# Kernel optimization log

Measured on AMD Instinct MI355X. Metric: run time of the kernel, lower is better.

## Reference

```python
import jax, jax.numpy as jnp
import numpy as np

KERNEL_MUL = 2.0
KERNEL_NUM = 5


def setup_inputs() -> dict:
    key = jax.random.key(0)
    k1, k2 = jax.random.split(key)
    source = jax.random.normal(k1, (4096, 256), dtype=jnp.float32)
    target = jax.random.normal(k2, (4096, 256), dtype=jnp.float32)
    return {"source": source, "target": target}


def _gaussian_mmd(source, target):
    n_src = source.shape[0]
    total = jnp.concatenate([source, target], axis=0)  # [n, d]
    n = total.shape[0]
    # pairwise squared L2 distances via the GEMM trick (equivalent to the
    # expand-based (total0 - total1)**2 sum in the original)
    sq = jnp.sum(total * total, axis=1)  # [n]
    l2 = jnp.maximum(sq[:, None] + sq[None, :] - 2.0 * (total @ total.T), 0.0)  # [n, n]
    # bandwidth from detached distances (torch uses .data -> stop_gradient)
    bandwidth = jax.lax.stop_gradient(jnp.sum(l2)) / (n * n - n)
    bandwidth = bandwidth / (KERNEL_MUL ** (KERNEL_NUM // 2))
    # multi-bandwidth gaussian kernel sum
    kernels = jnp.zeros_like(l2)
    for i in range(KERNEL_NUM):
        kernels = kernels + jnp.exp(-l2 / (bandwidth * KERNEL_MUL ** i))
    xx = jnp.mean(kernels[:n_src, :n_src])
    yy = jnp.mean(kernels[n_src:, n_src:])
    xy = jnp.mean(kernels[:n_src, n_src:])
    yx = jnp.mean(kernels[n_src:, :n_src])
    return xx + yy - xy - yx


def reference(source, target):
    return _gaussian_mmd(source, target)
```

## Files before the change

### kernel.cpp

```cpp
#include <hip/hip_runtime.h>

typedef float f32x4 __attribute__((ext_vector_type(4)));
typedef short bf16x8 __attribute__((ext_vector_type(8)));

#define N_TOTAL 8192
#define N_SRC   4096
#define DDIM    256
#define LOG2E   1.4426950408889634f

__device__ __forceinline__ unsigned short f2bf(float f) {
  return __builtin_bit_cast(unsigned short, (__bf16)f);
}

__global__ __launch_bounds__(256) void k_sq_cast(
    const float* __restrict__ src, const float* __restrict__ tgt,
    float* __restrict__ sq, unsigned short* __restrict__ Vbf,
    float* __restrict__ colsum) {
  const int t = threadIdx.x;
  const int lane = t & 63;
  const int w = t >> 6;
  const int row = blockIdx.x * 4 + w;
  const float* rowp = (row < N_SRC) ? (src + (size_t)row * DDIM)
                                    : (tgt + (size_t)(row - N_SRC) * DDIM);
  float4 v = ((const float4*)rowp)[lane];
  float ss = v.x * v.x + v.y * v.y + v.z * v.z + v.w * v.w;
  #pragma unroll
  for (int m = 32; m >= 1; m >>= 1) ss += __shfl_xor(ss, m, 64);
  if (lane == 0) sq[row] = ss;
  ushort4 p;
  p.x = f2bf(v.x); p.y = f2bf(v.y); p.z = f2bf(v.z); p.w = f2bf(v.w);
  ((ushort4*)Vbf)[(size_t)row * 64 + lane] = p;
  if (blockIdx.x == 0) colsum[t] = 0.0f;
}

__global__ __launch_bounds__(256) void k_colsum(
    const float* __restrict__ src, const float* __restrict__ tgt,
    float* __restrict__ colsum) {
  const int t = threadIdx.x;
  const int b = blockIdx.x;
  const float* base = (b < 32) ? (src + (size_t)b * 128 * DDIM)
                               : (tgt + (size_t)(b - 32) * 128 * DDIM);
  float p = 0.0f;
  for (int r = 0; r < 128; ++r) p += base[(size_t)r * DDIM + t];
  atomicAdd(colsum + t, p);
}

__global__ __launch_bounds__(256) void k_bw(
    const float* __restrict__ sq, const float* __restrict__ colsum,
    float* __restrict__ nc0, double* __restrict__ accum) {
  const int t = threadIdx.x;
  const int lane = t & 63;
  const int w = t >> 6;
  float sp = 0.0f;
  for (int i = t; i < N_TOTAL; i += 256) sp += sq[i];
  float c = colsum[t];
  float cp = c * c;
  #pragma unroll
  for (int m = 32; m >= 1; m >>= 1) {
    sp += __shfl_xor(sp, m, 64);
    cp += __shfl_xor(cp, m, 64);
  }
  __shared__ float red[8];
  if (lane == 0) { red[w] = sp; red[4 + w] = cp; }
  __syncthreads();
  if (t == 0) {
    float S   = red[0] + red[1] + red[2] + red[3];
    float CSQ = red[4] + red[5] + red[6] + red[7];
    float sum_l2 = 2.0f * (float)N_TOTAL * S - 2.0f * CSQ;
    float bw = sum_l2 / ((float)N_TOTAL * (float)N_TOTAL - (float)N_TOTAL) / 4.0f;
    *nc0 = -LOG2E / bw;
    *accum = 0.0;
  }
}

__global__ __launch_bounds__(256) void k_main(
    const unsigned short* __restrict__ Vbf, const float* __restrict__ sq,
    const float* __restrict__ nc0p, double* __restrict__ accum) {
  const int bcol = blockIdx.x;
  const int brow = blockIdx.y;
  if (bcol < brow) return;

  const int t = threadIdx.x;
  const int lane = t & 63;
  const int w = t >> 6;
  const int wr = w >> 1;
  const int wc = w & 1;
  const int i0 = brow * 128;
  const int j0 = bcol * 128;

  __shared__ uint4 lds4[2048];
  char* As = (char*)lds4;
  char* Bs = (char*)lds4 + 16384;

  const unsigned short* VA = Vbf + (size_t)i0 * DDIM;
  const unsigned short* VB = Vbf + (size_t)j0 * DDIM;

  f32x4 acc[4][4] = {};

  const int srow = t >> 3;
  const int scb  = (t & 7) * 16;

  for (int ks = 0; ks < 4; ++ks) {
    const int kc = ks * 64;
    __syncthreads();
    #pragma unroll
    for (int it = 0; it < 4; ++it) {
      const int r = it * 32 + srow;
      const int dst = r * 128 + (scb ^ ((r & 7) << 4));
      uint4 ga = *(const uint4*)(VA + (size_t)r * DDIM + kc + (scb >> 1));
      uint4 gb = *(const uint4*)(VB + (size_t)r * DDIM + kc + (scb >> 1));
      *(uint4*)(As + dst) = ga;
      *(uint4*)(Bs + dst) = gb;
    }
    __syncthreads();
    #pragma unroll
    for (int kk = 0; kk < 2; ++kk) {
      const int kbyte = kk * 64 + ((lane >> 4) << 4);
      bf16x8 a[4], b[4];
      #pragma unroll
      for (int m = 0; m < 4; ++m) {
        const int ra = wr * 64 + m * 16 + (lane & 15);
        a[m] = *(const bf16x8*)(As + ra * 128 + (kbyte ^ ((ra & 7) << 4)));
        const int rb = wc * 64 + m * 16 + (lane & 15);
        b[m] = *(const bf16x8*)(Bs + rb * 128 + (kbyte ^ ((rb & 7) << 4)));
      }
      #pragma unroll
      for (int m = 0; m < 4; ++m)
        #pragma unroll
        for (int n = 0; n < 4; ++n)
          acc[m][n] = __builtin_amdgcn_mfma_f32_16x16x32_bf16(a[m], b[n], acc[m][n], 0, 0, 0);
    }
  }

  const float nc0 = *nc0p;
  float rsv[16];
  const int rbase = i0 + wr * 64 + ((lane >> 4) << 2);
  #pragma unroll
  for (int m = 0; m < 4; ++m) {
    const float4 q = *(const float4*)(sq + rbase + m * 16);
    rsv[m * 4 + 0] = q.x; rsv[m * 4 + 1] = q.y;
    rsv[m * 4 + 2] = q.z; rsv[m * 4 + 3] = q.w;
  }
  float cs[4];
  const int cbase = j0 + wc * 64 + (lane & 15);
  #pragma unroll
  for (int n = 0; n < 4; ++n) cs[n] = sq[cbase + n * 16];

  float ksum = 0.0f;
  #pragma unroll
  for (int m = 0; m < 4; ++m)
    #pragma unroll
    for (int n = 0; n < 4; ++n)
      #pragma unroll
      for (int r = 0; r < 4; ++r) {
        const float g  = acc[m][n][r];
        const float l2 = fmaxf(fmaf(-2.0f, g, rsv[m * 4 + r]) + cs[n], 0.0f);
        const float tt = l2 * nc0;
        ksum += __builtin_amdgcn_exp2f(tt)
              + __builtin_amdgcn_exp2f(tt * 0.5f)
              + __builtin_amdgcn_exp2f(tt * 0.25f)
              + __builtin_amdgcn_exp2f(tt * 0.125f)
              + __builtin_amdgcn_exp2f(tt * 0.0625f);
      }

  #pragma unroll
  for (int m = 32; m >= 1; m >>= 1) ksum += __shfl_xor(ksum, m, 64);
  __shared__ float red[4];
  if (lane == 0) red[w] = ksum;
  __syncthreads();
  if (t == 0) {
    const float sign = ((brow < 32) == (bcol < 32)) ? 1.0f : -1.0f;
    const float mult = (brow == bcol) ? 1.0f : 2.0f;
    const double contrib = (double)((red[0] + red[1] + red[2] + red[3]) * sign * mult);
    atomicAdd(accum, contrib);
  }
}

__global__ void k_final(const double* __restrict__ accum, float* __restrict__ out) {
  out[0] = (float)(accum[0] * (1.0 / 16777216.0));
}

extern "C" void kernel_launch(void* const* d_in, const int* in_sizes, int n_in,
                              void* d_out, int out_size, void* d_ws, size_t ws_size,
                              hipStream_t stream) {
  const float* src = (const float*)d_in[0];
  const float* tgt = (const float*)d_in[1];
  char* ws = (char*)d_ws;
  double* accum          = (double*)ws;
  float*  nc0            = (float*)(ws + 8);
  float*  colsum         = (float*)(ws + 64);
  float*  sq             = (float*)(ws + 2048);
  unsigned short* Vbf    = (unsigned short*)(ws + 65536);
  float* out = (float*)d_out;

  hipLaunchKernelGGL(k_sq_cast, dim3(2048), dim3(256), 0, stream, src, tgt, sq, Vbf, colsum);
  hipLaunchKernelGGL(k_colsum,  dim3(64),   dim3(256), 0, stream, src, tgt, colsum);
  hipLaunchKernelGGL(k_bw,      dim3(1),    dim3(256), 0, stream, sq, colsum, nc0, accum);
  hipLaunchKernelGGL(k_main,    dim3(64, 64), dim3(256), 0, stream, Vbf, sq, nc0, accum);
  hipLaunchKernelGGL(k_final,   dim3(1),    dim3(1),   0, stream, accum, out);
}
```

Before: 133.8 us.

## Fuse prep kernels, compact triangular grid, square-chain exps, last-block finalize

Merges the square-norm/cast, column-sum and bandwidth kernels into one 64-block prep kernel that writes per-block column partials. Each main block now recomputes the bandwidth redundantly from those partials and sq. The main grid launches only the 2080 upper-triangle tiles, mapping block id to row and column with a sqrt formula. The five exp2 calls become one exp2 followed by repeated squaring. A done counter lets the last block write the output, which removes the final kernel. This cuts launch count, idle blocks and transcendental work, at the cost of redundant per-block reductions and a small change in rounding from the squaring chain.

Result: slower. 171.2 us (+27.9%).

```diff
diff --git a/kernel.cpp b/kernel.cpp
--- a/kernel.cpp
+++ b/kernel.cpp
@@ -1,183 +1,192 @@
 #include <hip/hip_runtime.h>
 
 typedef float f32x4 __attribute__((ext_vector_type(4)));
+typedef float f32x2 __attribute__((ext_vector_type(2)));
 typedef short bf16x8 __attribute__((ext_vector_type(8)));
 
-#define N_TOTAL 8192
-#define N_SRC   4096
-#define DDIM    256
-#define LOG2E   1.4426950408889634f
+#define LOG2E 1.4426950408889634f
 
 __device__ __forceinline__ unsigned short f2bf(float f) {
   return __builtin_bit_cast(unsigned short, (__bf16)f);
 }
 
-__global__ __launch_bounds__(256) void k_sq_cast(
+
+__global__ __launch_bounds__(256) void k_prep(
     const float* __restrict__ src, const float* __restrict__ tgt,
     float* __restrict__ sq, unsigned short* __restrict__ Vbf,
-    float* __restrict__ colsum) {
-  const int t = threadIdx.x;
-  const int lane = t & 63;
-  const int w = t >> 6;
-  const int row = blockIdx.x * 4 + w;
-  const float* rowp = (row < N_SRC) ? (src + (size_t)row * DDIM)
-                                    : (tgt + (size_t)(row - N_SRC) * DDIM);
-  float4 v = ((const float4*)rowp)[lane];
-  float ss = v.x * v.x + v.y * v.y + v.z * v.z + v.w * v.w;
-  #pragma unroll
-  for (int m = 32; m >= 1; m >>= 1) ss += __shfl_xor(ss, m, 64);
-  if (lane == 0) sq[row] = ss;
-  ushort4 p;
-  p.x = f2bf(v.x); p.y = f2bf(v.y); p.z = f2bf(v.z); p.w = f2bf(v.w);
-  ((ushort4*)Vbf)[(size_t)row * 64 + lane] = p;
-  if (blockIdx.x == 0) colsum[t] = 0.0f;
-}
-
-__global__ __launch_bounds__(256) void k_colsum(
-    const float* __restrict__ src, const float* __restrict__ tgt,
-    float* __restrict__ colsum) {
-  const int t = threadIdx.x;
-  const int b = blockIdx.x;
-  const float* base = (b < 32) ? (src + (size_t)b * 128 * DDIM)
-                               : (tgt + (size_t)(b - 32) * 128 * DDIM);
-  float p = 0.0f;
-  for (int r = 0; r < 128; ++r) p += base[(size_t)r * DDIM + t];
-  atomicAdd(colsum + t, p);
-}
-
-__global__ __launch_bounds__(256) void k_bw(
-    const float* __restrict__ sq, const float* __restrict__ colsum,
-    float* __restrict__ nc0, double* __restrict__ accum) {
-  const int t = threadIdx.x;
-  const int lane = t & 63;
-  const int w = t >> 6;
-  float sp = 0.0f;
-  for (int i = t; i < N_TOTAL; i += 256) sp += sq[i];
-  float c = colsum[t];
-  float cp = c * c;
-  #pragma unroll
-  for (int m = 32; m >= 1; m >>= 1) {
-    sp += __shfl_xor(sp, m, 64);
-    cp += __shfl_xor(cp, m, 64);
-  }
-  __shared__ float red[8];
-  if (lane == 0) { red[w] = sp; red[4 + w] = cp; }
+    float* __restrict__ partialT, double* __restrict__ accum,
+    unsigned int* __restrict__ done) {
+  const int t = threadIdx.x, lane = t & 63, w = t >> 6, b = blockIdx.x;
+  if (b == 0 && t == 0) { *accum = 0.0; *done = 0u; }
+  const int row0 = b * 128 + w * 32;
+  f32x4 colacc = {0.f, 0.f, 0.f, 0.f};
+  for (int i = 0; i < 32; ++i) {
+    const int row = row0 + i;
+    const float* rowp = (row < 4096) ? src + (size_t)row * 256
+                                     : tgt + (size_t)(row - 4096) * 256;
+    float4 v = ((const float4*)rowp)[lane];
+    colacc[0] += v.x; colacc[1] += v.y; colacc[2] += v.z; colacc[3] += v.w;
+    float ss = v.x * v.x + v.y * v.y + v.z * v.z + v.w * v.w;
+    #pragma unroll
+    for (int m = 32; m >= 1; m >>= 1) ss += __shfl_xor(ss, m, 64);
+    if (lane == 0) sq[row] = ss;
+    ushort4 p;
+    p.x = f2bf(v.x); p.y = f2bf(v.y); p.z = f2bf(v.z); p.w = f2bf(v.w);
+    ((ushort4*)Vbf)[(size_t)row * 64 + lane] = p;
+  }
+  __shared__ float cpart[4][256];
+  *(f32x4*)&cpart[w][lane * 4] = colacc;
   __syncthreads();
-  if (t == 0) {
-    float S   = red[0] + red[1] + red[2] + red[3];
-    float CSQ = red[4] + red[5] + red[6] + red[7];
-    float sum_l2 = 2.0f * (float)N_TOTAL * S - 2.0f * CSQ;
-    float bw = sum_l2 / ((float)N_TOTAL * (float)N_TOTAL - (float)N_TOTAL) / 4.0f;
-    *nc0 = -LOG2E / bw;
-    *accum = 0.0;
-  }
-}
-
-__global__ __launch_bounds__(256) void k_main(
+  const float pt = cpart[0][t] + cpart[1][t] + cpart[2][t] + cpart[3][t];
+  partialT[t * 64 + b] = pt;
+}
+
+__global__ __launch_bounds__(256, 4) void k_main(
     const unsigned short* __restrict__ Vbf, const float* __restrict__ sq,
-    const float* __restrict__ nc0p, double* __restrict__ accum) {
-  const int bcol = blockIdx.x;
-  const int brow = blockIdx.y;
-  if (bcol < brow) return;
+    const float* __restrict__ partialT, double* __restrict__ accum,
+    unsigned int* __restrict__ done, float* __restrict__ out) {
+  const int bid = blockIdx.x;
+  int r = (int)((129.0f - sqrtf(16641.0f - 8.0f * (float)bid)) * 0.5f);
+  int base = (r * (129 - r)) >> 1;
+  if (bid < base)                 { --r; base = (r * (129 - r)) >> 1; }
+  else if (bid - base >= 64 - r)  { ++r; base = (r * (129 - r)) >> 1; }
+  const int c = r + (bid - base);
+  const int i0 = r * 128;
+  const int j0 = c * 128;
 
   const int t = threadIdx.x;
   const int lane = t & 63;
   const int w = t >> 6;
   const int wr = w >> 1;
   const int wc = w & 1;
-  const int i0 = brow * 128;
-  const int j0 = bcol * 128;
 
   __shared__ uint4 lds4[2048];
   char* As = (char*)lds4;
   char* Bs = (char*)lds4 + 16384;
-
-  const unsigned short* VA = Vbf + (size_t)i0 * DDIM;
-  const unsigned short* VB = Vbf + (size_t)j0 * DDIM;
-
-  f32x4 acc[4][4] = {};
-
-  const int srow = t >> 3;
-  const int scb  = (t & 7) * 16;
-
-  for (int ks = 0; ks < 4; ++ks) {
-    const int kc = ks * 64;
+  float* redf = (float*)lds4;
+
+  float Sp = 0.f;
+  #pragma unroll
+  for (int j = 0; j < 8; ++j) {
+    float4 q = ((const float4*)sq)[t + 256 * j];
+    Sp += q.x + q.y + q.z + q.w;
+  }
+  float csum = 0.f;
+  #pragma unroll
+  for (int j = 0; j < 16; ++j) {
+    float4 q = ((const float4*)(partialT + t * 64))[j];
+    csum += q.x + q.y + q.z + q.w;
+  }
+  float Cp = csum * csum;
+  #pragma unroll
+  for (int m = 32; m >= 1; m >>= 1) {
+    Sp += __shfl_xor(Sp, m, 64);
+    Cp += __shfl_xor(Cp, m, 64);
+  }
+  if (lane == 0) { redf[w] = Sp; redf[4 + w] = Cp; }
+  __syncthreads();
+  {
+    const float S   = redf[0] + redf[1] + redf[2] + redf[3];
+    const float CSQ = redf[4] + redf[5] + redf[6] + redf[7];
+    const float sum_l2 = 2.f * 8192.f * S - 2.f * CSQ;
+    const float bw = sum_l2 / (8192.f * 8192.f - 8192.f) * 0.25f;
+    const float nc0s = -LOG2E / bw * 0.0625f;
+
+    const unsigned short* VA = Vbf + (size_t)i0 * 256;
+    const unsigned short* VB = Vbf + (size_t)j0 * 256;
+
+    f32x4 acc[4][4] = {};
+    const int srow = t >> 3;
+    const int scb  = (t & 7) * 16;
+
+    for (int ks = 0; ks < 4; ++ks) {
+      const int kc = ks * 64;
+      __syncthreads();
+      #pragma unroll
+      for (int it = 0; it < 4; ++it) {
+        const int rr = it * 32 + srow;
+        const int dst = rr * 128 + (scb ^ ((rr & 7) << 4));
+        uint4 ga = *(const uint4*)(VA + (size_t)rr * 256 + kc + (scb >> 1));
+        uint4 gb = *(const uint4*)(VB + (size_t)rr * 256 + kc + (scb >> 1));
+        *(uint4*)(As + dst) = ga;
+        *(uint4*)(Bs + dst) = gb;
+      }
+      __syncthreads();
+      #pragma unroll
+      for (int kk = 0; kk < 2; ++kk) {
+        const int kbyte = kk * 64 + ((lane >> 4) << 4);
+        bf16x8 a[4], b[4];
+        #pragma unroll
+        for (int m = 0; m < 4; ++m) {
+          const int ra = wr * 64 + m * 16 + (lane & 15);
+          a[m] = *(const bf16x8*)(As + ra * 128 + (kbyte ^ ((ra & 7) << 4)));
+          const int rb = wc * 64 + m * 16 + (lane & 15);
+          b[m] = *(const bf16x8*)(Bs + rb * 128 + (kbyte ^ ((rb & 7) << 4)));
+        }
+        #pragma unroll
+        for (int m = 0; m < 4; ++m)
+          #pragma unroll
+          for (int n = 0; n < 4; ++n)
+            acc[m][n] = __builtin_amdgcn_mfma_f32_16x16x32_bf16(a[m], b[n], acc[m][n], 0, 0, 0);
+      }
+    }
+
+    float rsv[16];
+    const int rbase = i0 + wr * 64 + ((lane >> 4) << 2);
+    #pragma unroll
+    for (int m = 0; m < 4; ++m) {
+      const float4 q = *(const float4*)(sq + rbase + m * 16);
+      rsv[m * 4 + 0] = q.x; rsv[m * 4 + 1] = q.y;
+      rsv[m * 4 + 2] = q.z; rsv[m * 4 + 3] = q.w;
+    }
+    float cs[4];
+    const int cbase = j0 + wc * 64 + (lane & 15);
+    #pragma unroll
+    for (int n = 0; n < 4; ++n) cs[n] = sq[cbase + n * 16];
+
+    f32x2 ks2 = {0.f, 0.f};
+    #pragma unroll
+    for (int m = 0; m < 4; ++m)
+      #pragma unroll
+      for (int n = 0; n < 4; ++n)
+        #pragma unroll
+        for (int h = 0; h < 2; ++h) {
+          f32x2 g  = { acc[m][n][2 * h], acc[m][n][2 * h + 1] };
+          f32x2 rc = { rsv[m * 4 + 2 * h] + cs[n], rsv[m * 4 + 2 * h + 1] + cs[n] };
+          f32x2 l2 = __builtin_elementwise_max(rc - 2.f * g, (f32x2){0.f, 0.f});
+          f32x2 tt = l2 * nc0s;
+          f32x2 e;
+          e[0] = __builtin_amdgcn_exp2f(tt[0]);
+          e[1] = __builtin_amdgcn_exp2f(tt[1]);
+          f32x2 s = e;
+          f32x2 e2 = e * e;   s += e2;
+          f32x2 e4 = e2 * e2; s += e4;
+          f32x2 e8 = e4 * e4; s += e8;
+          s += e8 * e8;
+          ks2 += s;
+        }
+    float ksum = ks2[0] + ks2[1];
+    #pragma unroll
+    for (int m = 32; m >= 1; m >>= 1) ksum += __shfl_xor(ksum, m, 64);
+
     __syncthreads();
-    #pragma unroll
-    for (int it = 0; it < 4; ++it) {
-      const int r = it * 32 + srow;
-      const int dst = r * 128 + (scb ^ ((r & 7) << 4));
-      uint4 ga = *(const uint4*)(VA + (size_t)r * DDIM + kc + (scb >> 1));
-      uint4 gb = *(const uint4*)(VB + (size_t)r * DDIM + kc + (scb >> 1));
-      *(uint4*)(As + dst) = ga;
-      *(uint4*)(Bs + dst) = gb;
+    if (lane == 0) redf[w] = ksum;
+    __syncthreads();
+    if (t == 0) {
+      const float sign = ((r < 32) == (c < 32)) ? 1.0f : -1.0f;
+      const float mult = (r == c) ? 1.0f : 2.0f;
+      const double contrib =
+          (double)((redf[0] + redf[1] + redf[2] + redf[3]) * sign * mult);
+      atomicAdd(accum, contrib);
+      __threadfence();
+      const unsigned int old = atomicAdd(done, 1u);
+      if (old == 2079u) {
+        __threadfence();
+        const double tot = atomicAdd(accum, 0.0);
+        out[0] = (float)(tot * (1.0 / 16777216.0));
+      }
     }
-    __syncthreads();
-    #pragma unroll
-    for (int kk = 0; kk < 2; ++kk) {
-      const int kbyte = kk * 64 + ((lane >> 4) << 4);
-      bf16x8 a[4], b[4];
-      #pragma unroll
-      for (int m = 0; m < 4; ++m) {
-        const int ra = wr * 64 + m * 16 + (lane & 15);
-        a[m] = *(const bf16x8*)(As + ra * 128 + (kbyte ^ ((ra & 7) << 4)));
-        const int rb = wc * 64 + m * 16 + (lane & 15);
-        b[m] = *(const bf16x8*)(Bs + rb * 128 + (kbyte ^ ((rb & 7) << 4)));
-      }
-      #pragma unroll
-      for (int m = 0; m < 4; ++m)
-        #pragma unroll
-        for (int n = 0; n < 4; ++n)
-          acc[m][n] = __builtin_amdgcn_mfma_f32_16x16x32_bf16(a[m], b[n], acc[m][n], 0, 0, 0);
-    }
-  }
-
-  const float nc0 = *nc0p;
-  float rsv[16];
-  const int rbase = i0 + wr * 64 + ((lane >> 4) << 2);
-  #pragma unroll
-  for (int m = 0; m < 4; ++m) {
-    const float4 q = *(const float4*)(sq + rbase + m * 16);
-    rsv[m * 4 + 0] = q.x; rsv[m * 4 + 1] = q.y;
-    rsv[m * 4 + 2] = q.z; rsv[m * 4 + 3] = q.w;
-  }
-  float cs[4];
-  const int cbase = j0 + wc * 64 + (lane & 15);
-  #pragma unroll
-  for (int n = 0; n < 4; ++n) cs[n] = sq[cbase + n * 16];
-
-  float ksum = 0.0f;
-  #pragma unroll
-  for (int m = 0; m < 4; ++m)
-    #pragma unroll
-    for (int n = 0; n < 4; ++n)
-      #pragma unroll
-      for (int r = 0; r < 4; ++r) {
-        const float g  = acc[m][n][r];
-        const float l2 = fmaxf(fmaf(-2.0f, g, rsv[m * 4 + r]) + cs[n], 0.0f);
-        const float tt = l2 * nc0;
-        ksum += __builtin_amdgcn_exp2f(tt)
-              + __builtin_amdgcn_exp2f(tt * 0.5f)
-              + __builtin_amdgcn_exp2f(tt * 0.25f)
-              + __builtin_amdgcn_exp2f(tt * 0.125f)
-              + __builtin_amdgcn_exp2f(tt * 0.0625f);
-      }
-
-  #pragma unroll
-  for (int m = 32; m >= 1; m >>= 1) ksum += __shfl_xor(ksum, m, 64);
-  __shared__ float red[4];
-  if (lane == 0) red[w] = ksum;
-  __syncthreads();
-  if (t == 0) {
-    const float sign = ((brow < 32) == (bcol < 32)) ? 1.0f : -1.0f;
-    const float mult = (brow == bcol) ? 1.0f : 2.0f;
-    const double contrib = (double)((red[0] + red[1] + red[2] + red[3]) * sign * mult);
-    atomicAdd(accum, contrib);
-  }
-}
-
-__global__ void k_final(const double* __restrict__ accum, float* __restrict__ out) {
-  out[0] = (float)(accum[0] * (1.0 / 16777216.0));
+  }
 }
 
 extern "C" void kernel_launch(void* const* d_in, const int* in_sizes, int n_in,
@@ -186,16 +195,15 @@
   const float* src = (const float*)d_in[0];
   const float* tgt = (const float*)d_in[1];
   char* ws = (char*)d_ws;
-  double* accum          = (double*)ws;
-  float*  nc0            = (float*)(ws + 8);
-  float*  colsum         = (float*)(ws + 64);
-  float*  sq             = (float*)(ws + 2048);
-  unsigned short* Vbf    = (unsigned short*)(ws + 65536);
+  double*         accum    = (double*)ws;
+  unsigned int*   done     = (unsigned int*)(ws + 16);
+  float*          partialT = (float*)(ws + 1024);
+  float*          sq       = (float*)(ws + 66560);
+  unsigned short* Vbf      = (unsigned short*)(ws + 131072);
   float* out = (float*)d_out;
 
-  hipLaunchKernelGGL(k_sq_cast, dim3(2048), dim3(256), 0, stream, src, tgt, sq, Vbf, colsum);
-  hipLaunchKernelGGL(k_colsum,  dim3(64),   dim3(256), 0, stream, src, tgt, colsum);
-  hipLaunchKernelGGL(k_bw,      dim3(1),    dim3(256), 0, stream, sq, colsum, nc0, accum);
-  hipLaunchKernelGGL(k_main,    dim3(64, 64), dim3(256), 0, stream, Vbf, sq, nc0, accum);
-  hipLaunchKernelGGL(k_final,   dim3(1),    dim3(1),   0, stream, accum, out);
-}
+  hipLaunchKernelGGL(k_prep, dim3(64),   dim3(256), 0, stream,
+                     src, tgt, sq, Vbf, partialT, accum, done);
+  hipLaunchKernelGGL(k_main, dim3(2080), dim3(256), 0, stream,
+                     Vbf, sq, partialT, accum, done, out);
+}
```
